# Optimization experiments

Hardware: AMD Instinct MI355X
Metric: run time of the kernel (lower is better)

The kernel has to match this reference:

```python
import jax, jax.numpy as jnp
import numpy as np

B, T, D = 8, 8192, 256
H = 16            # history_length
K = 3             # neighbor kernel_size
DECAY = 0.9
EPS = 1e-5


def _layernorm(x, g, b):
    m = jnp.mean(x, axis=-1, keepdims=True)
    v = jnp.var(x, axis=-1, keepdims=True)
    return (x - m) * jax.lax.rsqrt(v + EPS) * g + b


def _window_weighted_sum(x_pad, weights, seq_len):
    # sum_j w[j] * x_pad[:, j:j+T, :] -- fixed-weight local aggregation,
    # avoids materializing the [B,T,W,D] unfold tensor.
    out = weights[0] * x_pad[:, 0:seq_len, :]
    for j in range(1, weights.shape[0]):
        out = out + weights[j] * x_pad[:, j:j + seq_len, :]
    return out


def temporal_weights():
    w = DECAY ** np.arange(H, dtype=np.float32)
    return jnp.asarray(w / w.sum())


def setup_inputs() -> dict:
    key = jax.random.key(0)
    ks = jax.random.split(key, 16)
    s = 1.0 / np.sqrt(D)
    s2 = 1.0 / np.sqrt(2 * D)
    inp = {
        "x": jax.random.normal(ks[0], (B, T, D), jnp.float32),
        # LayerNorms
        "n1_g": jnp.ones((D,), jnp.float32), "n1_b": jnp.zeros((D,), jnp.float32),
        "n2_g": jnp.ones((D,), jnp.float32), "n2_b": jnp.zeros((D,), jnp.float32),
        "n3_g": jnp.ones((D,), jnp.float32), "n3_b": jnp.zeros((D,), jnp.float32),
        # temporal value/out proj (stored as [in,out])
        "t_Wv": jax.random.uniform(ks[1], (D, D), jnp.float32, -s, s),
        "t_bv": jax.random.uniform(ks[2], (D,), jnp.float32, -s, s),
        "t_Wo": jax.random.uniform(ks[3], (D, D), jnp.float32, -s, s),
        "t_bo": jax.random.uniform(ks[4], (D,), jnp.float32, -s, s),
        # neighbor value/out proj
        "a_Wv": jax.random.uniform(ks[5], (D, D), jnp.float32, -s, s),
        "a_bv": jax.random.uniform(ks[6], (D,), jnp.float32, -s, s),
        "a_Wo": jax.random.uniform(ks[7], (D, D), jnp.float32, -s, s),
        "a_bo": jax.random.uniform(ks[8], (D,), jnp.float32, -s, s),
        # FFN
        "f_W1": jax.random.uniform(ks[9], (D, 2 * D), jnp.float32, -s, s),
        "f_b1": jax.random.uniform(ks[10], (2 * D,), jnp.float32, -s, s),
        "f_W2": jax.random.uniform(ks[11], (2 * D, D), jnp.float32, -s2, s2),
        "f_b2": jax.random.uniform(ks[12], (D,), jnp.float32, -s2, s2),
    }
    return inp


def reference(x, n1_g, n1_b, n2_g, n2_b, n3_g, n3_b,
              t_Wv, t_bv, t_Wo, t_bo,
              a_Wv, a_bv, a_Wo, a_bo,
              f_W1, f_b1, f_W2, f_b2):
    # --- temporal memory: causal fixed exponential-decay window ---
    h = _layernorm(x, n1_g, n1_b)
    h_pad = jnp.pad(h, ((0, 0), (H - 1, 0), (0, 0)))  # zeros on the left
    tw = temporal_weights()  # tw[j] weights the j-th-oldest element (decay^j)
    agg = _window_weighted_sum(h_pad, tw, T)
    # weights sum to 1 => weighted-sum-of-linear == linear-of-weighted-sum
    attended = agg @ t_Wv + t_bv
    x = x + (attended @ t_Wo + t_bo)

    # --- neighbor attention: [t-1, t, t+1] uniform window, replicate pad ---
    h = _layernorm(x, n2_g, n2_b)
    h_pad = jnp.pad(h, ((0, 0), (1, 1), (0, 0)), mode="edge")
    nw = jnp.full((K,), 1.0 / K, jnp.float32)
    agg = _window_weighted_sum(h_pad, nw, T)
    attended = agg @ a_Wv + a_bv
    x = x + (attended @ a_Wo + a_bo)

    # --- FFN (dropout is identity at eval) ---
    h = _layernorm(x, n3_g, n3_b)
    h = jax.nn.gelu(h @ f_W1 + f_b1, approximate=False)
    x = x + (h @ f_W2 + f_b2)
    return x
```

## Files before the change

### kernel.cpp

```cpp
#include <hip/hip_runtime.h>
#include <cstdint>
#include <cstddef>

#define TT 8192
#define BB 8
#define DD 256
#define NTOK (BB * TT)

typedef unsigned short u16;
typedef unsigned int u32;

typedef __attribute__((ext_vector_type(8))) short bf16x8;
typedef __attribute__((ext_vector_type(4))) float f32x4;

__device__ __forceinline__ float bf2f(u16 u) {
    u32 v = ((u32)u) << 16;
    float f;
    __builtin_memcpy(&f, &v, 4);
    return f;
}

__device__ __forceinline__ u16 f2bf(float f) {
    u32 v;
    __builtin_memcpy(&v, &f, 4);
    u32 r = (v + 0x7FFFu + ((v >> 16) & 1u)) >> 16;
    return (u16)r;
}

__device__ __forceinline__ uint2 pack4(const float* v) {
    uint2 p;
    p.x = (u32)f2bf(v[0]) | ((u32)f2bf(v[1]) << 16);
    p.y = (u32)f2bf(v[2]) | ((u32)f2bf(v[3]) << 16);
    return p;
}

__device__ __forceinline__ void unpack4(uint2 p, float* v) {
    v[0] = bf2f((u16)(p.x & 0xFFFFu));
    v[1] = bf2f((u16)(p.x >> 16));
    v[2] = bf2f((u16)(p.y & 0xFFFFu));
    v[3] = bf2f((u16)(p.y >> 16));
}

__device__ __forceinline__ uint4 pack8(const float* v) {
    uint4 p;
    p.x = (u32)f2bf(v[0]) | ((u32)f2bf(v[1]) << 16);
    p.y = (u32)f2bf(v[2]) | ((u32)f2bf(v[3]) << 16);
    p.z = (u32)f2bf(v[4]) | ((u32)f2bf(v[5]) << 16);
    p.w = (u32)f2bf(v[6]) | ((u32)f2bf(v[7]) << 16);
    return p;
}

__device__ __forceinline__ void unpack8(uint4 p, float* v) {
    v[0] = bf2f((u16)(p.x & 0xFFFFu));
    v[1] = bf2f((u16)(p.x >> 16));
    v[2] = bf2f((u16)(p.y & 0xFFFFu));
    v[3] = bf2f((u16)(p.y >> 16));
    v[4] = bf2f((u16)(p.z & 0xFFFFu));
    v[5] = bf2f((u16)(p.z >> 16));
    v[6] = bf2f((u16)(p.w & 0xFFFFu));
    v[7] = bf2f((u16)(p.w >> 16));
}

__global__ __launch_bounds__(256) void k_diag(float* out, float code) {
    out[(size_t)blockIdx.x * 256 + threadIdx.x] = code;
}

__global__ __launch_bounds__(256) void k_transpose(
    const float* s0, const float* s1, const float* s2, const float* s3,
    const float* s4, const float* s5,
    u16* d0, u16* d1, u16* d2, u16* d3, u16* d4, u16* d5) {
    const int z = blockIdx.z;
    const float* src;
    u16* dst;
    int K, N, tr;
    switch (z) {
        case 0: src = s0; dst = d0; K = 256; N = 256; tr = 1; break;
        case 1: src = s1; dst = d1; K = 256; N = 256; tr = 1; break;
        case 2: src = s2; dst = d2; K = 256; N = 512; tr = 1; break;
        case 3: src = s3; dst = d3; K = 512; N = 256; tr = 1; break;
        case 4: src = s4; dst = d4; K = 256; N = 256; tr = 0; break;
        default: src = s5; dst = d5; K = 256; N = 256; tr = 0; break;
    }
    const int nb = blockIdx.x * 32, kb = blockIdx.y * 32;
    if (nb >= N || kb >= K) return;
    const int tx = threadIdx.x & 31, ty = threadIdx.x >> 5;
    if (!tr) {
        for (int i = ty; i < 32; i += 8)
            dst[(size_t)(kb + i) * N + nb + tx] =
                f2bf(src[(size_t)(kb + i) * N + nb + tx]);
        return;
    }
    __shared__ u16 tile[32][33];
    for (int i = ty; i < 32; i += 8)
        tile[i][tx] = f2bf(src[(size_t)(kb + i) * N + nb + tx]);
    __syncthreads();
    for (int i = ty; i < 32; i += 8)
        dst[(size_t)(nb + i) * K + kb + tx] = tile[tx][i];
}

__global__ __launch_bounds__(256) void k_bias_compose(
    const float* tbv, const float* tWo, const float* tbo,
    const float* abv, const float* aWo, const float* abo,
    float* bc1, float* bc2) {
    const float* bv = blockIdx.x ? abv : tbv;
    const float* Wo = blockIdx.x ? aWo : tWo;
    const float* bo = blockIdx.x ? abo : tbo;
    float* bc = blockIdx.x ? bc2 : bc1;
    const int n = threadIdx.x;
    float s = bo[n];
    for (int j = 0; j < 256; j++) s += bv[j] * Wo[j * 256 + n];
    bc[n] = s;
}

__global__ __launch_bounds__(256) void k_gemm_prep(
    const u16* __restrict__ A, const u16* __restrict__ Wt,
    u16* out, int M, int K, int Nc, int ldw) {
    const int m0 = blockIdx.y * 128;
    const int n0 = blockIdx.x * 128;
    const int tid = threadIdx.x;
    const int wv = tid >> 6, lane = tid & 63;
    const int quad = lane >> 4, l16 = lane & 15;
    const int wm = (wv >> 1) * 64, wn = (wv & 1) * 64;

    __shared__ u16 lA[128 * 40];
    __shared__ u16 lB[128 * 40];

    f32x4 acc[4][4];
#pragma unroll
    for (int i = 0; i < 4; i++)
#pragma unroll
        for (int j = 0; j < 4; j++) acc[i][j] = (f32x4){0.f, 0.f, 0.f, 0.f};

    const int r = tid >> 2;
    const int c = tid & 3;

    for (int k0 = 0; k0 < K; k0 += 32) {
        __syncthreads();
        {
            const uint4 a0 = *(const uint4*)(A + (size_t)(m0 + r) * K + k0 + c * 8);
            const uint4 a1 = *(const uint4*)(A + (size_t)(m0 + r + 64) * K + k0 + c * 8);
            const uint4 b0 = *(const uint4*)(Wt + (size_t)(n0 + r) * ldw + k0 + c * 8);
            const uint4 b1 = *(const uint4*)(Wt + (size_t)(n0 + r + 64) * ldw + k0 + c * 8);
            *(uint4*)(lA + r * 40 + c * 8) = a0;
            *(uint4*)(lA + (r + 64) * 40 + c * 8) = a1;
            *(uint4*)(lB + r * 40 + c * 8) = b0;
            *(uint4*)(lB + (r + 64) * 40 + c * 8) = b1;
        }
        __syncthreads();
        bf16x8 af[4], bfr[4];
#pragma unroll
        for (int i = 0; i < 4; i++)
            af[i] = *(const bf16x8*)(lA + (wm + i * 16 + l16) * 40 + quad * 8);
#pragma unroll
        for (int j = 0; j < 4; j++)
            bfr[j] = *(const bf16x8*)(lB + (wn + j * 16 + l16) * 40 + quad * 8);
#pragma unroll
        for (int i = 0; i < 4; i++)
#pragma unroll
            for (int j = 0; j < 4; j++)
                acc[i][j] = __builtin_amdgcn_mfma_f32_16x16x32_bf16(
                    af[i], bfr[j], acc[i][j], 0, 0, 0);
    }

#pragma unroll
    for (int i = 0; i < 4; i++) {
        const int rowb = m0 + wm + i * 16 + quad * 4;
#pragma unroll
        for (int j = 0; j < 4; j++) {
            const int col = n0 + wn + j * 16 + l16;
#pragma unroll
            for (int rr = 0; rr < 4; rr++)
                out[(size_t)(rowb + rr) * Nc + col] = f2bf(acc[i][j][rr]);
        }
    }
}

__global__ __launch_bounds__(256) void k_p12(
    const float* __restrict__ x, const float* __restrict__ n1g,
    const float* __restrict__ n1b, const u16* __restrict__ Wt,
    const float* __restrict__ bias, float* outf,
    const float* __restrict__ lng, const float* __restrict__ lnb,
    u16* __restrict__ hout) {
    const int b = blockIdx.y;
    const int t0 = blockIdx.x * 64;
    const size_t base = (size_t)b * TT;
    const int t = threadIdx.x;
    const int lane = t & 63, wv = t >> 6;
    const int quad = lane >> 4, l16 = lane & 15;
    const int wn = wv * 64;

    __shared__ __attribute__((aligned(16))) u16 hl[79 * 256];
    __shared__ __attribute__((aligned(16))) u16 sAg[64 * 264];
    float* sE = (float*)hl;
    __shared__ float sMean[16], sRstd[16];
    __shared__ float sG[256], sBl[256];

    sG[t] = lng[t];
    sBl[t] = lnb[t];

    const int d4 = lane * 4;
    {
        const float4 gv = *(const float4*)(n1g + d4);
        const float4 bv = *(const float4*)(n1b + d4);
        for (int i = wv; i < 79; i += 4) {
            const int tt = t0 + i - 15;
            if (tt < 0) {
                *(uint2*)(hl + i * 256 + d4) = make_uint2(0u, 0u);
                continue;
            }
            const float4 v = *(const float4*)(x + (base + tt) * DD + d4);
            float s = v.x + v.y + v.z + v.w;
            float ss = v.x * v.x + v.y * v.y + v.z * v.z + v.w * v.w;
            for (int m = 1; m < 64; m <<= 1) {
                s += __shfl_xor(s, m);
                ss += __shfl_xor(ss, m);
            }
            const float mean = s * (1.0f / 256.0f);
            const float var = ss * (1.0f / 256.0f) - mean * mean;
            const float rs = rsqrtf(fmaxf(var, 0.f) + 1e-5f);
            float h[4] = {(v.x - mean) * rs * gv.x + bv.x,
                          (v.y - mean) * rs * gv.y + bv.y,
                          (v.z - mean) * rs * gv.z + bv.z,
                          (v.w - mean) * rs * gv.w + bv.w};
            *(uint2*)(hl + i * 256 + d4) = pack4(h);
        }
    }
    __syncthreads();

    {
        float tw[16];
        float p = 1.f, s = 0.f;
        for (int j = 0; j < 16; j++) {
            tw[j] = p;
            s += p;
            p *= 0.9f;
        }
        const float inv = 1.f / s;
        for (int j = 0; j < 16; j++) tw[j] *= inv;
        const int tg = wv * 16;
        for (int ot = tg; ot < tg + 16; ++ot) {
            float a[4] = {0.f, 0.f, 0.f, 0.f};
            for (int j = 0; j < 16; j++) {
                float h[4];
                unpack4(*(const uint2*)(hl + (ot + j) * 256 + d4), h);
                a[0] += tw[j] * h[0];
                a[1] += tw[j] * h[1];
                a[2] += tw[j] * h[2];
                a[3] += tw[j] * h[3];
            }
            *(uint2*)(sAg + ot * 264 + d4) = pack4(a);
        }
    }
    __syncthreads();

    f32x4 acc[4][4];
#pragma unroll
    for (int i = 0; i < 4; i++)
#pragma unroll
        for (int j = 0; j < 4; j++) acc[i][j] = (f32x4){0.f, 0.f, 0.f, 0.f};
#pragma unroll
    for (int ks = 0; ks < 8; ks++) {
        bf16x8 bfr[4], af[4];
#pragma unroll
        for (int j = 0; j < 4; j++)
            bfr[j] = *(const bf16x8*)(Wt + (size_t)(wn + j * 16 + l16) * 256 +
                                      ks * 32 + quad * 8);
#pragma unroll
        for (int i = 0; i < 4; i++)
            af[i] = *(const bf16x8*)(sAg + (i * 16 + l16) * 264 + ks * 32 +
                                     quad * 8);
#pragma unroll
        for (int i = 0; i < 4; i++)
#pragma unroll
            for (int j = 0; j < 4; j++)
                acc[i][j] = __builtin_amdgcn_mfma_f32_16x16x32_bf16(
                    af[i], bfr[j], acc[i][j], 0, 0, 0);
    }

    float bvl[4];
#pragma unroll
    for (int j = 0; j < 4; j++) bvl[j] = bias[wn + j * 16 + l16];

    const int row = t >> 4;
    const int colb = (t & 15) * 16;
    for (int cch = 0; cch < 4; cch++) {
        const size_t grow = base + t0 + cch * 16 + row;
        __syncthreads();
        {
            const float* rp = x + grow * 256 + colb;
            float* sp = sE + row * 268 + colb;
#pragma unroll
            for (int q = 0; q < 4; q++)
                *(float4*)(sp + q * 4) = *(const float4*)(rp + q * 4);
        }
        __syncthreads();
#pragma unroll
        for (int j = 0; j < 4; j++) {
#pragma unroll
            for (int rr = 0; rr < 4; rr++) {
                const int rl = quad * 4 + rr;
                const int ad = rl * 268 + wn + j * 16 + l16;
                sE[ad] += acc[cch][j][rr] + bvl[j];
            }
        }
        __syncthreads();
#pragma unroll
        for (int r4 = 0; r4 < 4; r4++) {
            const int rl = wv * 4 + r4;
            const float4 vv = *(const float4*)(sE + rl * 268 + lane * 4);
            float s = vv.x + vv.y + vv.z + vv.w;
            float ss = vv.x * vv.x + vv.y * vv.y + vv.z * vv.z + vv.w * vv.w;
            for (int m = 1; m < 64; m <<= 1) {
                s += __shfl_xor(s, m);
                ss += __shfl_xor(ss, m);
            }
            if (lane == 0) {
                const float mean = s * (1.0f / 256.0f);
                const float var = ss * (1.0f / 256.0f) - mean * mean;
                sMean[rl] = mean;
                sRstd[rl] = rsqrtf(fmaxf(var, 0.f) + 1e-5f);
            }
        }
        __syncthreads();
        const float* sp = sE + row * 268 + colb;
        {
            float* op = outf + grow * 256 + colb;
#pragma unroll
            for (int q = 0; q < 4; q++)
                *(float4*)(op + q * 4) = *(const float4*)(sp + q * 4);
        }
        {
            const float m = sMean[row], rs = sRstd[row];
            float h[16];
#pragma unroll
            for (int e = 0; e < 16; e++)
                h[e] = (sp[e] - m) * rs * sG[colb + e] + sBl[colb + e];
            u16* hp = hout + grow * 256 + colb;
            *(uint4*)hp = pack8(h);
            *(uint4*)(hp + 8) = pack8(h + 8);
        }
    }
}

template <int AMODE>
__global__ __launch_bounds__(256) void k_mega2(
    const u16* __restrict__ A,
    const u16* __restrict__ Wt,
    const float* __restrict__ bias,
    const float* res,
    float* outf,
    const float* __restrict__ lng, const float* __restrict__ lnb,
    u16* __restrict__ hout) {
    const int m0 = blockIdx.x * 64;
    const int t = threadIdx.x;
    const int lane = t & 63, wv = t >> 6;
    const int quad = lane >> 4, l16 = lane & 15;
    const int wn = wv * 64;

    __shared__ __attribute__((aligned(16))) u16 sA[8 * 64 * 40];
    float* sE = (float*)sA;
    __shared__ float sMean[16], sRstd[16];
    __shared__ float sG[256], sBl[256];

    sG[t] = lng[t];
    sBl[t] = lnb[t];

#pragma unroll
    for (int q = 0; q < 8; q++) {
        const int id = q * 256 + t;
        const int arow = id >> 5;
        const int c8 = (id & 31) * 8;
        const int ks = c8 >> 5;
        const int kc = c8 & 31;
        const int gr = m0 + arow;
        if (AMODE == 0) {
            *(uint4*)(sA + (ks * 64 + arow) * 40 + kc) =
                *(const uint4*)(A + (size_t)gr * 256 + c8);
        } else {
            const int rm = ((gr & (TT - 1)) == 0) ? gr : gr - 1;
            const int rp = (((gr + 1) & (TT - 1)) == 0) ? gr : gr + 1;
            float v0[8], v1[8], v2[8], o[8];
            unpack8(*(const uint4*)(A + (size_t)rm * 256 + c8), v0);
            unpack8(*(const uint4*)(A + (size_t)gr * 256 + c8), v1);
            unpack8(*(const uint4*)(A + (size_t)rp * 256 + c8), v2);
#pragma unroll
            for (int e = 0; e < 8; e++)
                o[e] = (v0[e] + v1[e] + v2[e]) * (1.0f / 3.0f);
            *(uint4*)(sA + (ks * 64 + arow) * 40 + kc) = pack8(o);
        }
    }

    f32x4 acc[4][4];
#pragma unroll
    for (int i = 0; i < 4; i++)
#pragma unroll
        for (int j = 0; j < 4; j++) acc[i][j] = (f32x4){0.f, 0.f, 0.f, 0.f};

    __syncthreads();

#pragma unroll
    for (int ks = 0; ks < 8; ks++) {
        bf16x8 bfr[4], af[4];
#pragma unroll
        for (int j = 0; j < 4; j++)
            bfr[j] = *(const bf16x8*)(Wt + (size_t)(wn + j * 16 + l16) * 256 +
                                      ks * 32 + quad * 8);
#pragma unroll
        for (int i = 0; i < 4; i++)
            af[i] = *(const bf16x8*)(sA + (ks * 64 + i * 16 + l16) * 40 +
                                     quad * 8);
#pragma unroll
        for (int i = 0; i < 4; i++)
#pragma unroll
            for (int j = 0; j < 4; j++)
                acc[i][j] = __builtin_amdgcn_mfma_f32_16x16x32_bf16(
                    af[i], bfr[j], acc[i][j], 0, 0, 0);
    }

    float bvl[4];
#pragma unroll
    for (int j = 0; j < 4; j++) bvl[j] = bias[wn + j * 16 + l16];

    const int row = t >> 4;
    const int colb = (t & 15) * 16;
    for (int cch = 0; cch < 4; cch++) {
        const int gr = m0 + cch * 16 + row;
        __syncthreads();
        {
            const float* rp = res + (size_t)gr * 256 + colb;
            float* sp = sE + row * 268 + colb;
#pragma unroll
            for (int q = 0; q < 4; q++)
                *(float4*)(sp + q * 4) = *(const float4*)(rp + q * 4);
        }
        __syncthreads();
#pragma unroll
        for (int j = 0; j < 4; j++) {
#pragma unroll
            for (int rr = 0; rr < 4; rr++) {
                const int rl = quad * 4 + rr;
                const int ad = rl * 268 + wn + j * 16 + l16;
                sE[ad] += acc[cch][j][rr] + bvl[j];
            }
        }
        __syncthreads();
#pragma unroll
        for (int r4 = 0; r4 < 4; r4++) {
            const int rl = wv * 4 + r4;
            const float4 vv = *(const float4*)(sE + rl * 268 + lane * 4);
            float s = vv.x + vv.y + vv.z + vv.w;
            float ss = vv.x * vv.x + vv.y * vv.y + vv.z * vv.z + vv.w * vv.w;
            for (int m = 1; m < 64; m <<= 1) {
                s += __shfl_xor(s, m);
                ss += __shfl_xor(ss, m);
            }
            if (lane == 0) {
                const float mean = s * (1.0f / 256.0f);
                const float var = ss * (1.0f / 256.0f) - mean * mean;
                sMean[rl] = mean;
                sRstd[rl] = rsqrtf(fmaxf(var, 0.f) + 1e-5f);
            }
        }
        __syncthreads();
        const float* sp = sE + row * 268 + colb;
        {
            float* op = outf + (size_t)gr * 256 + colb;
#pragma unroll
            for (int q = 0; q < 4; q++)
                *(float4*)(op + q * 4) = *(const float4*)(sp + q * 4);
        }
        {
            const float m = sMean[row], rs = sRstd[row];
            float h[16];
#pragma unroll
            for (int e = 0; e < 16; e++)
                h[e] = (sp[e] - m) * rs * sG[colb + e] + sBl[colb + e];
            u16* hp = hout + (size_t)gr * 256 + colb;
            *(uint4*)hp = pack8(h);
            *(uint4*)(hp + 8) = pack8(h + 8);
        }
    }
}

__global__ __launch_bounds__(256) void k_ffn(
    const u16* __restrict__ A,
    const u16* __restrict__ W1T,
    const float* __restrict__ b1,
    const u16* __restrict__ W2T,
    const float* __restrict__ b2,
    const float* res,
    float* out) {
    const int m0 = blockIdx.x * 64;
    const int t = threadIdx.x;
    const int lane = t & 63, wv = t >> 6;
    const int quad = lane >> 4, l16 = lane & 15;

    __shared__ __attribute__((aligned(16))) u16 sA[8 * 64 * 40];
    __shared__ __attribute__((aligned(16))) u16 sT[64 * 72];
    float* sE = (float*)sA;

#pragma unroll
    for (int q = 0; q < 8; q++) {
        const int id = q * 256 + t;
        const int arow = id >> 5;
        const int c8 = (id & 31) * 8;
        const int ks = c8 >> 5;
        const int kc = c8 & 31;
        *(uint4*)(sA + (ks * 64 + arow) * 40 + kc) =
            *(const uint4*)(A + (size_t)(m0 + arow) * 256 + c8);
    }

    f32x4 acc2[4][4];
#pragma unroll
    for (int i = 0; i < 4; i++)
#pragma unroll
        for (int jj = 0; jj < 4; jj++) acc2[i][jj] = (f32x4){0.f, 0.f, 0.f, 0.f};

    __syncthreads();

    for (int j = 0; j < 8; j++) {
        bf16x8 bw2[8];
#pragma unroll
        for (int kh = 0; kh < 2; kh++)
#pragma unroll
            for (int jj = 0; jj < 4; jj++)
                bw2[kh * 4 + jj] = *(const bf16x8*)(
                    W2T + (size_t)(wv * 64 + jj * 16 + l16) * 512 + j * 64 +
                    kh * 32 + quad * 8);
        const int n1 = j * 64 + wv * 16 + l16;
        bf16x8 bw[8];
#pragma unroll
        for (int ks = 0; ks < 8; ks++)
            bw[ks] = *(const bf16x8*)(W1T + (size_t)n1 * 256 + ks * 32 + quad * 8);
        f32x4 acc1[4];
#pragma unroll
        for (int i = 0; i < 4; i++) acc1[i] = (f32x4){0.f, 0.f, 0.f, 0.f};
#pragma unroll
        for (int ks = 0; ks < 8; ks++) {
#pragma unroll
            for (int i = 0; i < 4; i++) {
                const bf16x8 af = *(const bf16x8*)(
                    sA + (ks * 64 + i * 16 + l16) * 40 + quad * 8);
                acc1[i] = __builtin_amdgcn_mfma_f32_16x16x32_bf16(
                    af, bw[ks], acc1[i], 0, 0, 0);
            }
        }
        const float b1l = b1[n1];
#pragma unroll
        for (int i = 0; i < 4; i++)
#pragma unroll
            for (int rr = 0; rr < 4; rr++) {
                float v = acc1[i][rr] + b1l;
                v = 0.5f * v * (1.0f + erff(v * 0.70710678118654752f));
                sT[(i * 16 + quad * 4 + rr) * 72 + wv * 16 + l16] = f2bf(v);
            }
        __syncthreads();
#pragma unroll
        for (int kh = 0; kh < 2; kh++) {
#pragma unroll
            for (int i = 0; i < 4; i++) {
                const bf16x8 af = *(const bf16x8*)(
                    sT + (i * 16 + l16) * 72 + kh * 32 + quad * 8);
#pragma unroll
                for (int jj = 0; jj < 4; jj++)
                    acc2[i][jj] = __builtin_amdgcn_mfma_f32_16x16x32_bf16(
                        af, bw2[kh * 4 + jj], acc2[i][jj], 0, 0, 0);
            }
        }
        __syncthreads();
    }

    float bvl[4];
#pragma unroll
    for (int jj = 0; jj < 4; jj++) bvl[jj] = b2[wv * 64 + jj * 16 + l16];
    const int row = t >> 4;
    const int colb = (t & 15) * 16;
    for (int cch = 0; cch < 4; cch++) {
        const int gr = m0 + cch * 16 + row;
        __syncthreads();
        {
            const float* rp = res + (size_t)gr * 256 + colb;
            float* sp = sE + row * 268 + colb;
#pragma unroll
            for (int q = 0; q < 4; q++)
                *(float4*)(sp + q * 4) = *(const float4*)(rp + q * 4);
        }
        __syncthreads();
#pragma unroll
        for (int jj = 0; jj < 4; jj++)
#pragma unroll
            for (int rr = 0; rr < 4; rr++) {
                const int ad = (quad * 4 + rr) * 268 + wv * 64 + jj * 16 + l16;
                sE[ad] += acc2[cch][jj][rr] + bvl[jj];
            }
        __syncthreads();
        {
            float* op = out + (size_t)gr * 256 + colb;
            const float* sp = sE + row * 268 + colb;
#pragma unroll
            for (int q = 0; q < 4; q++)
                *(float4*)(op + q * 4) = *(const float4*)(sp + q * 4);
        }
    }
}

extern "C" void kernel_launch(void* const* d_in, const int* in_sizes, int n_in,
                              void* d_out, int out_size, void* d_ws,
                              size_t ws_size, hipStream_t stream) {
    const float* x = (const float*)d_in[0];
    const float* n1g = (const float*)d_in[1];
    const float* n1b = (const float*)d_in[2];
    const float* n2g = (const float*)d_in[3];
    const float* n2b = (const float*)d_in[4];
    const float* n3g = (const float*)d_in[5];
    const float* n3b = (const float*)d_in[6];
    const float* tWv = (const float*)d_in[7];
    const float* tbv = (const float*)d_in[8];
    const float* tWo = (const float*)d_in[9];
    const float* tbo = (const float*)d_in[10];
    const float* aWv = (const float*)d_in[11];
    const float* abv = (const float*)d_in[12];
    const float* aWo = (const float*)d_in[13];
    const float* abo = (const float*)d_in[14];
    const float* fW1 = (const float*)d_in[15];
    const float* fb1 = (const float*)d_in[16];
    const float* fW2 = (const float*)d_in[17];
    const float* fb2 = (const float*)d_in[18];
    float* outp = (float*)d_out;

    u16* wq = (u16*)d_ws;
    u16* tWoT = wq;
    u16* aWoT = wq + 65536;
    u16* fW1T = wq + 131072;
    u16* fW2T = wq + 262144;
    u16* WcT1 = wq + 393216;
    u16* WcT2 = wq + 458752;
    u16* tWvB = wq + 524288;
    u16* aWvB = wq + 589824;
    float* bc1 = (float*)(wq + 655360);
    float* bc2 = (float*)(wq + 655872);
    const size_t W_ELEMS = 656384;
    const size_t SLOT = (size_t)NTOK * 256;
    u16* slot1 = wq + W_ELEMS;
    u16* slot2 = slot1 + SLOT;
    u16* slot3 = slot2 + SLOT;
    (void)slot3;

    const size_t need = (W_ELEMS + 3 * SLOT) * 2;
    if (ws_size < need) {
        k_diag<<<dim3(NTOK), 256, 0, stream>>>(outp,
                                               512.0f + (float)(ws_size >> 20));
        return;
    }

    k_transpose<<<dim3(16, 16, 6), 256, 0, stream>>>(
        tWo, aWo, fW1, fW2, tWv, aWv, tWoT, aWoT, fW1T, fW2T, tWvB, aWvB);
    k_gemm_prep<<<dim3(2, 2), 256, 0, stream>>>(tWoT, tWvB, WcT1, 256, 256,
                                                256, 256);
    k_gemm_prep<<<dim3(2, 2), 256, 0, stream>>>(aWoT, aWvB, WcT2, 256, 256,
                                                256, 256);
    k_bias_compose<<<dim3(2), 256, 0, stream>>>(tbv, tWo, tbo, abv, aWo, abo,
                                                bc1, bc2);

    const dim3 mg(NTOK / 64);

    k_p12<<<dim3(TT / 64, BB), 256, 0, stream>>>(x, n1g, n1b, WcT1, bc1, outp,
                                                 n2g, n2b, slot2);

    k_mega2<1><<<mg, 256, 0, stream>>>(slot2, WcT2, bc2, outp, outp, n3g, n3b,
                                       slot1);

    k_ffn<<<mg, 256, 0, stream>>>(slot1, fW1T, fb1, fW2T, fb2, outp, outp);
}
```

Before: 399.0 us.

## Fuse neighbor-attention and FFN kernels, merge prep launches, use recursive decay sum

```diff
diff --git a/kernel.cpp b/kernel.cpp
--- a/kernel.cpp
+++ b/kernel.cpp
@@ -68,8 +68,22 @@
 __global__ __launch_bounds__(256) void k_transpose(
     const float* s0, const float* s1, const float* s2, const float* s3,
     const float* s4, const float* s5,
-    u16* d0, u16* d1, u16* d2, u16* d3, u16* d4, u16* d5) {
+    u16* d0, u16* d1, u16* d2, u16* d3, u16* d4, u16* d5,
+    const float* tbv, const float* tbo, const float* abv, const float* abo,
+    float* bc1, float* bc2) {
     const int z = blockIdx.z;
+    if (z >= 6) {
+        if (blockIdx.x || blockIdx.y) return;
+        const float* bv = (z == 7) ? abv : tbv;
+        const float* Wo = (z == 7) ? s1 : s0;
+        const float* bo = (z == 7) ? abo : tbo;
+        float* bc = (z == 7) ? bc2 : bc1;
+        const int n = threadIdx.x;
+        float s = bo[n];
+        for (int j = 0; j < 256; j++) s += bv[j] * Wo[j * 256 + n];
+        bc[n] = s;
+        return;
+    }
     const float* src;
     u16* dst;
     int K, N, tr;
@@ -98,23 +112,12 @@
         dst[(size_t)(nb + i) * K + kb + tx] = tile[tx][i];
 }
 
-__global__ __launch_bounds__(256) void k_bias_compose(
-    const float* tbv, const float* tWo, const float* tbo,
-    const float* abv, const float* aWo, const float* abo,
-    float* bc1, float* bc2) {
-    const float* bv = blockIdx.x ? abv : tbv;
-    const float* Wo = blockIdx.x ? aWo : tWo;
-    const float* bo = blockIdx.x ? abo : tbo;
-    float* bc = blockIdx.x ? bc2 : bc1;
-    const int n = threadIdx.x;
-    float s = bo[n];
-    for (int j = 0; j < 256; j++) s += bv[j] * Wo[j * 256 + n];
-    bc[n] = s;
-}
-
 __global__ __launch_bounds__(256) void k_gemm_prep(
-    const u16* __restrict__ A, const u16* __restrict__ Wt,
-    u16* out, int M, int K, int Nc, int ldw) {
+    const u16* __restrict__ A0, const u16* __restrict__ B0, u16* O0,
+    const u16* __restrict__ A1, const u16* __restrict__ B1, u16* O1) {
+    const u16* A = blockIdx.z ? A1 : A0;
+    const u16* Wt = blockIdx.z ? B1 : B0;
+    u16* out = blockIdx.z ? O1 : O0;
     const int m0 = blockIdx.y * 128;
     const int n0 = blockIdx.x * 128;
     const int tid = threadIdx.x;
@@ -134,13 +137,13 @@
     const int r = tid >> 2;
     const int c = tid & 3;
 
-    for (int k0 = 0; k0 < K; k0 += 32) {
-        __syncthreads();
-        {
-            const uint4 a0 = *(const uint4*)(A + (size_t)(m0 + r) * K + k0 + c * 8);
-            const uint4 a1 = *(const uint4*)(A + (size_t)(m0 + r + 64) * K + k0 + c * 8);
-            const uint4 b0 = *(const uint4*)(Wt + (size_t)(n0 + r) * ldw + k0 + c * 8);
-            const uint4 b1 = *(const uint4*)(Wt + (size_t)(n0 + r + 64) * ldw + k0 + c * 8);
+    for (int k0 = 0; k0 < 256; k0 += 32) {
+        __syncthreads();
+        {
+            const uint4 a0 = *(const uint4*)(A + (size_t)(m0 + r) * 256 + k0 + c * 8);
+            const uint4 a1 = *(const uint4*)(A + (size_t)(m0 + r + 64) * 256 + k0 + c * 8);
+            const uint4 b0 = *(const uint4*)(Wt + (size_t)(n0 + r) * 256 + k0 + c * 8);
+            const uint4 b1 = *(const uint4*)(Wt + (size_t)(n0 + r + 64) * 256 + k0 + c * 8);
             *(uint4*)(lA + r * 40 + c * 8) = a0;
             *(uint4*)(lA + (r + 64) * 40 + c * 8) = a1;
             *(uint4*)(lB + r * 40 + c * 8) = b0;
@@ -170,7 +173,7 @@
             const int col = n0 + wn + j * 16 + l16;
 #pragma unroll
             for (int rr = 0; rr < 4; rr++)
-                out[(size_t)(rowb + rr) * Nc + col] = f2bf(acc[i][j][rr]);
+                out[(size_t)(rowb + rr) * 256 + col] = f2bf(acc[i][j][rr]);
         }
     }
 }
@@ -228,26 +231,38 @@
     __syncthreads();
 
     {
-        float tw[16];
-        float p = 1.f, s = 0.f;
+        float p = 1.f, s = 0.f, w15 = 1.f;
         for (int j = 0; j < 16; j++) {
-            tw[j] = p;
             s += p;
+            if (j == 15) w15 = p;
             p *= 0.9f;
         }
-        const float inv = 1.f / s;
-        for (int j = 0; j < 16; j++) tw[j] *= inv;
+        const float c = 1.f / s;
+        const float inv09 = 1.0f / 0.9f;
         const int tg = wv * 16;
-        for (int ot = tg; ot < tg + 16; ++ot) {
-            float a[4] = {0.f, 0.f, 0.f, 0.f};
-            for (int j = 0; j < 16; j++) {
-                float h[4];
-                unpack4(*(const uint2*)(hl + (ot + j) * 256 + d4), h);
-                a[0] += tw[j] * h[0];
-                a[1] += tw[j] * h[1];
-                a[2] += tw[j] * h[2];
-                a[3] += tw[j] * h[3];
-            }
+        float g[4] = {0.f, 0.f, 0.f, 0.f};
+        float pw = 1.f;
+        for (int j = 0; j < 16; j++) {
+            float h[4];
+            unpack4(*(const uint2*)(hl + (tg + j) * 256 + d4), h);
+            g[0] += pw * h[0];
+            g[1] += pw * h[1];
+            g[2] += pw * h[2];
+            g[3] += pw * h[3];
+            pw *= 0.9f;
+        }
+        {
+            float a[4] = {c * g[0], c * g[1], c * g[2], c * g[3]};
+            *(uint2*)(sAg + tg * 264 + d4) = pack4(a);
+        }
+        for (int ot = tg + 1; ot < tg + 16; ++ot) {
+            float hold[4], hnew[4];
+            unpack4(*(const uint2*)(hl + (ot - 1) * 256 + d4), hold);
+            unpack4(*(const uint2*)(hl + (ot + 15) * 256 + d4), hnew);
+#pragma unroll
+            for (int e = 0; e < 4; e++)
+                g[e] = (g[e] - hold[e]) * inv09 + w15 * hnew[e];
+            float a[4] = {c * g[0], c * g[1], c * g[2], c * g[3]};
             *(uint2*)(sAg + ot * 264 + d4) = pack4(a);
         }
     }
@@ -342,15 +357,17 @@
     }
 }
 
-template <int AMODE>
-__global__ __launch_bounds__(256) void k_mega2(
-    const u16* __restrict__ A,
-    const u16* __restrict__ Wt,
-    const float* __restrict__ bias,
-    const float* res,
-    float* outf,
-    const float* __restrict__ lng, const float* __restrict__ lnb,
-    u16* __restrict__ hout) {
+__global__ __launch_bounds__(256) void k_p3f(
+    const u16* __restrict__ h2,
+    const u16* __restrict__ Wc2T,
+    const float* __restrict__ bc2,
+    const float* r1,
+    const float* __restrict__ n3g, const float* __restrict__ n3b,
+    const u16* __restrict__ W1T,
+    const float* __restrict__ b1,
+    const u16* __restrict__ W2T,
+    const float* __restrict__ b2,
+    float* out) {
     const int m0 = blockIdx.x * 64;
     const int t = threadIdx.x;
     const int lane = t & 63, wv = t >> 6;
@@ -358,12 +375,13 @@
     const int wn = wv * 64;
 
     __shared__ __attribute__((aligned(16))) u16 sA[8 * 64 * 40];
-    float* sE = (float*)sA;
+    __shared__ __attribute__((aligned(16))) float sE[16 * 268];
+    __shared__ __attribute__((aligned(16))) u16 sT[64 * 72];
+    __shared__ float sG[256], sBl[256];
     __shared__ float sMean[16], sRstd[16];
-    __shared__ float sG[256], sBl[256];
-
-    sG[t] = lng[t];
-    sBl[t] = lnb[t];
+
+    sG[t] = n3g[t];
+    sBl[t] = n3b[t];
 
 #pragma unroll
     for (int q = 0; q < 8; q++) {
@@ -373,21 +391,16 @@
         const int ks = c8 >> 5;
         const int kc = c8 & 31;
         const int gr = m0 + arow;
-        if (AMODE == 0) {
-            *(uint4*)(sA + (ks * 64 + arow) * 40 + kc) =
-                *(const uint4*)(A + (size_t)gr * 256 + c8);
-        } else {
-            const int rm = ((gr & (TT - 1)) == 0) ? gr : gr - 1;
-            const int rp = (((gr + 1) & (TT - 1)) == 0) ? gr : gr + 1;
-            float v0[8], v1[8], v2[8], o[8];
-            unpack8(*(const uint4*)(A + (size_t)rm * 256 + c8), v0);
-            unpack8(*(const uint4*)(A + (size_t)gr * 256 + c8), v1);
-            unpack8(*(const uint4*)(A + (size_t)rp * 256 + c8), v2);
-#pragma unroll
-            for (int e = 0; e < 8; e++)
-                o[e] = (v0[e] + v1[e] + v2[e]) * (1.0f / 3.0f);
-            *(uint4*)(sA + (ks * 64 + arow) * 40 + kc) = pack8(o);
-        }
+        const int rm = ((gr & (TT - 1)) == 0) ? gr : gr - 1;
+        const int rp = (((gr + 1) & (TT - 1)) == 0) ? gr : gr + 1;
+        float v0[8], v1[8], v2[8], o[8];
+        unpack8(*(const uint4*)(h2 + (size_t)rm * 256 + c8), v0);
+        unpack8(*(const uint4*)(h2 + (size_t)gr * 256 + c8), v1);
+        unpack8(*(const uint4*)(h2 + (size_t)rp * 256 + c8), v2);
+#pragma unroll
+        for (int e = 0; e < 8; e++)
+            o[e] = (v0[e] + v1[e] + v2[e]) * (1.0f / 3.0f);
+        *(uint4*)(sA + (ks * 64 + arow) * 40 + kc) = pack8(o);
     }
 
     f32x4 acc[4][4];
@@ -403,7 +416,7 @@
         bf16x8 bfr[4], af[4];
 #pragma unroll
         for (int j = 0; j < 4; j++)
-            bfr[j] = *(const bf16x8*)(Wt + (size_t)(wn + j * 16 + l16) * 256 +
+            bfr[j] = *(const bf16x8*)(Wc2T + (size_t)(wn + j * 16 + l16) * 256 +
                                       ks * 32 + quad * 8);
 #pragma unroll
         for (int i = 0; i < 4; i++)
@@ -417,17 +430,17 @@
                     af[i], bfr[j], acc[i][j], 0, 0, 0);
     }
 
-    float bvl[4];
-#pragma unroll
-    for (int j = 0; j < 4; j++) bvl[j] = bias[wn + j * 16 + l16];
+    float bvl2[4];
+#pragma unroll
+    for (int j = 0; j < 4; j++) bvl2[j] = bc2[wn + j * 16 + l16];
 
     const int row = t >> 4;
     const int colb = (t & 15) * 16;
+
     for (int cch = 0; cch < 4; cch++) {
-        const int gr = m0 + cch * 16 + row;
-        __syncthreads();
-        {
-            const float* rp = res + (size_t)gr * 256 + colb;
+        __syncthreads();
+        {
+            const float* rp = r1 + (size_t)(m0 + cch * 16 + row) * 256 + colb;
             float* sp = sE + row * 268 + colb;
 #pragma unroll
             for (int q = 0; q < 4; q++)
@@ -438,9 +451,10 @@
         for (int j = 0; j < 4; j++) {
 #pragma unroll
             for (int rr = 0; rr < 4; rr++) {
-                const int rl = quad * 4 + rr;
-                const int ad = rl * 268 + wn + j * 16 + l16;
-                sE[ad] += acc[cch][j][rr] + bvl[j];
+                const int ad = (quad * 4 + rr) * 268 + wn + j * 16 + l16;
+                const float v = sE[ad] + acc[cch][j][rr] + bvl2[j];
+                acc[cch][j][rr] = v;
+                sE[ad] = v;
             }
         }
         __syncthreads();
@@ -462,61 +476,26 @@
             }
         }
         __syncthreads();
-        const float* sp = sE + row * 268 + colb;
-        {
-            float* op = outf + (size_t)gr * 256 + colb;
-#pragma unroll
-            for (int q = 0; q < 4; q++)
-                *(float4*)(op + q * 4) = *(const float4*)(sp + q * 4);
-        }
         {
             const float m = sMean[row], rs = sRstd[row];
+            const float* sp = sE + row * 268 + colb;
             float h[16];
 #pragma unroll
             for (int e = 0; e < 16; e++)
                 h[e] = (sp[e] - m) * rs * sG[colb + e] + sBl[colb + e];
-            u16* hp = hout + (size_t)gr * 256 + colb;
-            *(uint4*)hp = pack8(h);
-            *(uint4*)(hp + 8) = pack8(h + 8);
-        }
-    }
-}
-
-__global__ __launch_bounds__(256) void k_ffn(
-    const u16* __restrict__ A,
-    const u16* __restrict__ W1T,
-    const float* __restrict__ b1,
-    const u16* __restrict__ W2T,
-    const float* __restrict__ b2,
-    const float* res,
-    float* out) {
-    const int m0 = blockIdx.x * 64;
-    const int t = threadIdx.x;
-    const int lane = t & 63, wv = t >> 6;
-    const int quad = lane >> 4, l16 = lane & 15;
-
-    __shared__ __attribute__((aligned(16))) u16 sA[8 * 64 * 40];
-    __shared__ __attribute__((aligned(16))) u16 sT[64 * 72];
-    float* sE = (float*)sA;
-
-#pragma unroll
-    for (int q = 0; q < 8; q++) {
-        const int id = q * 256 + t;
-        const int arow = id >> 5;
-        const int c8 = (id & 31) * 8;
-        const int ks = c8 >> 5;
-        const int kc = c8 & 31;
-        *(uint4*)(sA + (ks * 64 + arow) * 40 + kc) =
-            *(const uint4*)(A + (size_t)(m0 + arow) * 256 + c8);
-    }
+            const int ks = colb >> 5, kc = colb & 31;
+            const int r3 = cch * 16 + row;
+            *(uint4*)(sA + (ks * 64 + r3) * 40 + kc) = pack8(h);
+            *(uint4*)(sA + (ks * 64 + r3) * 40 + kc + 8) = pack8(h + 8);
+        }
+    }
+    __syncthreads();
 
     f32x4 acc2[4][4];
 #pragma unroll
     for (int i = 0; i < 4; i++)
 #pragma unroll
         for (int jj = 0; jj < 4; jj++) acc2[i][jj] = (f32x4){0.f, 0.f, 0.f, 0.f};
-
-    __syncthreads();
 
     for (int j = 0; j < 8; j++) {
         bf16x8 bw2[8];
@@ -525,7 +504,7 @@
 #pragma unroll
             for (int jj = 0; jj < 4; jj++)
                 bw2[kh * 4 + jj] = *(const bf16x8*)(
-                    W2T + (size_t)(wv * 64 + jj * 16 + l16) * 512 + j * 64 +
+                    W2T + (size_t)(wn + jj * 16 + l16) * 512 + j * 64 +
                     kh * 32 + quad * 8);
         const int n1 = j * 64 + wv * 16 + l16;
         bf16x8 bw[8];
@@ -572,30 +551,19 @@
 
     float bvl[4];
 #pragma unroll
-    for (int jj = 0; jj < 4; jj++) bvl[jj] = b2[wv * 64 + jj * 16 + l16];
-    const int row = t >> 4;
-    const int colb = (t & 15) * 16;
+    for (int jj = 0; jj < 4; jj++) bvl[jj] = b2[wn + jj * 16 + l16];
     for (int cch = 0; cch < 4; cch++) {
-        const int gr = m0 + cch * 16 + row;
-        __syncthreads();
-        {
-            const float* rp = res + (size_t)gr * 256 + colb;
-            float* sp = sE + row * 268 + colb;
-#pragma unroll
-            for (int q = 0; q < 4; q++)
-                *(float4*)(sp + q * 4) = *(const float4*)(rp + q * 4);
-        }
         __syncthreads();
 #pragma unroll
         for (int jj = 0; jj < 4; jj++)
 #pragma unroll
             for (int rr = 0; rr < 4; rr++) {
-                const int ad = (quad * 4 + rr) * 268 + wv * 64 + jj * 16 + l16;
-                sE[ad] += acc2[cch][jj][rr] + bvl[jj];
-            }
-        __syncthreads();
-        {
-            float* op = out + (size_t)gr * 256 + colb;
+                const int ad = (quad * 4 + rr) * 268 + wn + jj * 16 + l16;
+                sE[ad] = acc[cch][jj][rr] + acc2[cch][jj][rr] + bvl[jj];
+            }
+        __syncthreads();
+        {
+            float* op = out + (size_t)(m0 + cch * 16 + row) * 256 + colb;
             const float* sp = sE + row * 268 + colb;
 #pragma unroll
             for (int q = 0; q < 4; q++)
@@ -643,8 +611,7 @@
     const size_t SLOT = (size_t)NTOK * 256;
     u16* slot1 = wq + W_ELEMS;
     u16* slot2 = slot1 + SLOT;
-    u16* slot3 = slot2 + SLOT;
-    (void)slot3;
+    (void)slot1;
 
     const size_t need = (W_ELEMS + 3 * SLOT) * 2;
     if (ws_size < need) {
@@ -653,22 +620,16 @@
         return;
     }
 
-    k_transpose<<<dim3(16, 16, 6), 256, 0, stream>>>(
-        tWo, aWo, fW1, fW2, tWv, aWv, tWoT, aWoT, fW1T, fW2T, tWvB, aWvB);
-    k_gemm_prep<<<dim3(2, 2), 256, 0, stream>>>(tWoT, tWvB, WcT1, 256, 256,
-                                                256, 256);
-    k_gemm_prep<<<dim3(2, 2), 256, 0, stream>>>(aWoT, aWvB, WcT2, 256, 256,
-                                                256, 256);
-    k_bias_compose<<<dim3(2), 256, 0, stream>>>(tbv, tWo, tbo, abv, aWo, abo,
-                                                bc1, bc2);
-
-    const dim3 mg(NTOK / 64);
+    k_transpose<<<dim3(16, 16, 8), 256, 0, stream>>>(
+        tWo, aWo, fW1, fW2, tWv, aWv, tWoT, aWoT, fW1T, fW2T, tWvB, aWvB,
+        tbv, tbo, abv, abo, bc1, bc2);
+    k_gemm_prep<<<dim3(2, 2, 2), 256, 0, stream>>>(tWoT, tWvB, WcT1, aWoT,
+                                                   aWvB, WcT2);
 
     k_p12<<<dim3(TT / 64, BB), 256, 0, stream>>>(x, n1g, n1b, WcT1, bc1, outp,
                                                  n2g, n2b, slot2);
 
-    k_mega2<1><<<mg, 256, 0, stream>>>(slot2, WcT2, bc2, outp, outp, n3g, n3b,
-                                       slot1);
-
-    k_ffn<<<mg, 256, 0, stream>>>(slot1, fW1T, fb1, fW2T, fb2, outp, outp);
-}
+    k_p3f<<<dim3(NTOK / 64), 256, 0, stream>>>(slot2, WcT2, bc2, outp, n3g,
+                                               n3b, fW1T, fb1, fW2T, fb2,
+                                               outp);
+}
```

Result: slower. 435.5 us (+9.1%).
